# Optimization experiments

Hardware: AMD Instinct MI355X
Metric: run time of the kernel (lower is better)

## Reference

```python
import jax, jax.numpy as jnp
import numpy as np

D_IN, D_HEAD, D_EXPAND, D_OUT, H = 512, 64, 2048, 512, 8
D_Q = D_HEAD * H  # 512
D_K = D_HEAD * H  # 512
D_V = D_IN * H    # 4096 (non-standard: per-head value dim = d_in)
EPS = 1e-5


def layernorm(x, g, b):
    mu = jnp.mean(x, axis=-1, keepdims=True)
    var = jnp.mean(jnp.square(x - mu), axis=-1, keepdims=True)
    return (x - mu) * jax.lax.rsqrt(var + EPS) * g + b


def setup_inputs() -> dict:
    key = jax.random.key(0)
    ks = jax.random.split(key, 12)
    B, N = 2, 2048
    s_in = 1.0 / np.sqrt(D_IN)
    s_mh = 1.0 / np.sqrt(D_IN * H)
    s_ex = 1.0 / np.sqrt(D_EXPAND)
    return {
        "x": jax.random.normal(ks[0], (B, N, D_IN), jnp.float32),
        "ln1_g": jnp.ones((D_IN,), jnp.float32),
        "ln1_b": jnp.zeros((D_IN,), jnp.float32),
        "Wqkv": jax.random.normal(ks[1], (D_IN, D_Q + D_K + D_V), jnp.float32) * s_in,
        "bqkv": jax.random.normal(ks[2], (D_Q + D_K + D_V,), jnp.float32) * 0.01,
        "Wm": jax.random.normal(ks[3], (D_IN * H, D_IN), jnp.float32) * s_mh,
        "bm": jax.random.normal(ks[4], (D_IN,), jnp.float32) * 0.01,
        "ln2_g": jnp.ones((D_IN,), jnp.float32),
        "ln2_b": jnp.zeros((D_IN,), jnp.float32),
        "W1": jax.random.normal(ks[5], (D_IN, D_EXPAND), jnp.float32) * s_in,
        "b1": jax.random.normal(ks[6], (D_EXPAND,), jnp.float32) * 0.01,
        "W2": jax.random.normal(ks[7], (D_EXPAND, D_OUT), jnp.float32) * s_ex,
        "b2": jax.random.normal(ks[8], (D_OUT,), jnp.float32) * 0.01,
    }


def reference(x, ln1_g, ln1_b, Wqkv, bqkv, Wm, bm, ln2_g, ln2_b, W1, b1, W2, b2):
    B, N, _ = x.shape
    scale = D_HEAD ** -0.5
    qkv = layernorm(x, ln1_g, ln1_b) @ Wqkv + bqkv
    q, k, v = jnp.split(qkv, [D_Q, D_Q + D_K], axis=-1)
    q = q.reshape(B, N, H, D_HEAD).transpose(0, 2, 1, 3)  # (B,H,N,dh)
    k = k.reshape(B, N, H, D_HEAD).transpose(0, 2, 1, 3)
    v = v.reshape(B, N, H, D_IN).transpose(0, 2, 1, 3)    # (B,H,N,d_in)
    attn = jax.nn.softmax(jnp.einsum('bhnd,bhmd->bhnm', q, k) * scale, axis=-1)
    out = jnp.einsum('bhnm,bhmc->bhnc', attn, v)          # (B,H,N,d_in)
    out = out.transpose(0, 2, 1, 3).reshape(B, N, H * D_IN)
    x2 = x + out @ Wm + bm
    h = layernorm(x2, ln2_g, ln2_b) @ W1 + b1
    h = h * jax.nn.sigmoid(h)  # Swish
    return h @ W2 + b2 + x2    # shortcut = Identity (d_in == d_out)
```

## Files before the change

### kernel.cpp

```cpp
#include <hip/hip_runtime.h>
#include <cmath>

typedef unsigned short u16;
typedef unsigned int   u32;
typedef __attribute__((ext_vector_type(8))) __bf16 bf16x8;
typedef __attribute__((ext_vector_type(4))) float  f32x4;
typedef __attribute__((ext_vector_type(8))) unsigned short u16x8;
typedef __attribute__((ext_vector_type(4))) unsigned short u16x4;

#define DEV __device__ __forceinline__

DEV float bf2f(u16 u){ union{u32 i; float f;} v; v.i=((u32)u)<<16; return v.f; }
DEV u16 f2bf(float f){ union{float f; u32 i;} v; v.f=f; u32 r=v.i+0x7fffu+((v.i>>16)&1u); return (u16)(r>>16); }

#if defined(__has_builtin) && __has_builtin(__builtin_amdgcn_global_load_lds)
DEV void gld16(const void* g, void* l){
  __builtin_amdgcn_global_load_lds((__attribute__((address_space(1))) void*)g,
                                   (__attribute__((address_space(3))) void*)l, 16, 0, 0);
}
#else
DEV void gld16(const void* g, void* l){ *(u16x8*)l = *(const u16x8*)g; }
#endif

#if defined(__has_builtin) && __has_builtin(__builtin_amdgcn_exp2f)
DEV float fexp2(float x){ return __builtin_amdgcn_exp2f(x); }
#else
DEV float fexp2(float x){ return exp2f(x); }
#endif

__global__ void detect_k(const u16* __restrict__ x, int* __restrict__ flag)
{
  if (threadIdx.x == 0 && blockIdx.x == 0){
    int sane = 0;
    for (int i = 0; i < 64; ++i){
      int e = (x[i] >> 7) & 0xFF;
      sane += (e >= 100 && e <= 150);
    }
    *flag = (sane < 56) ? 1 : 0;
  }
}

__global__ __launch_bounds__(256)
void conv_vecs(const void* a0,const void* a1,const void* a2,const void* a3,
               const void* a4,const void* a5,const void* a6,const void* a7,
               float* __restrict__ dst, const int* __restrict__ flag)
{
  int i = blockIdx.x*256 + threadIdx.x;
  if (i >= 10240) return;
  const void* src; int off;
  if      (i < 512)  { src=a0; off=i; }
  else if (i < 1024) { src=a1; off=i-512; }
  else if (i < 6144) { src=a2; off=i-1024; }
  else if (i < 6656) { src=a3; off=i-6144; }
  else if (i < 7168) { src=a4; off=i-6656; }
  else if (i < 7680) { src=a5; off=i-7168; }
  else if (i < 9728) { src=a6; off=i-7680; }
  else               { src=a7; off=i-9728; }
  dst[i] = (*flag) ? ((const float*)src)[off] : bf2f(((const u16*)src)[off]);
}

#define SWZ_SRC(c) (((c)&7) ^ (((c)>>3)&7))

template<int SWZ>
DEV void remap_xcd(int& bx, int& by)
{
  if (SWZ==1){
    int L = by*(int)gridDim.x + bx;
    int xcd = L & 7, l = L >> 3;
    int chunk = (int)gridDim.x >> 3;
    bx = xcd*chunk + (l % chunk);
    by = l / chunk;
  } else if (SWZ==2){
    int L = by*(int)gridDim.x + bx;
    int xcd = L & 7, l = L >> 3;
    int chunk = (int)gridDim.y >> 3;
    by = xcd*chunk + (l % chunk);
    bx = l / chunk;
  }
}

template<int MODE, int SWZ, bool VT>
__global__ __launch_bounds__(256)
void gemm_bt(const u16* __restrict__ A, const u16* __restrict__ BT,
             void* __restrict__ C, const float* __restrict__ bias,
             int K, int lda, int ldb, int ldc, u16* __restrict__ vout)
{
  __shared__ u16 AB[2*128*64];
  u16* As = AB;
  u16* Bs = AB + 128*64;
  const int tid  = threadIdx.x;
  const int lane = tid & 63;
  const int quad = lane>>4, l7 = lane&7, l15 = lane&15;
  const int wv   = tid >> 6;
  const int wm   = wv >> 1, wn = wv & 1;
  int bx = blockIdx.x, by = blockIdx.y;
  remap_xcd<SWZ>(bx, by);
  const long m0 = (long)by * 128;
  const long n0 = (long)bx * 128;

  f32x4 acc[4][4];
#pragma unroll
  for (int i=0;i<4;i++)
#pragma unroll
    for (int j=0;j<4;j++) acc[i][j] = (f32x4){0.f,0.f,0.f,0.f};

  for (int k0=0; k0<K; k0+=64){
    __syncthreads();
#pragma unroll
    for (int i=0;i<4;i++){
      int c = i*256 + tid;
      gld16(A  + (m0 + (c>>3))*lda + k0 + SWZ_SRC(c)*8, &As[c*8]);
      gld16(BT + (n0 + (c>>3))*ldb + k0 + SWZ_SRC(c)*8, &Bs[c*8]);
    }
    __syncthreads();
#pragma unroll
    for (int kk=0;kk<2;kk++){
      const int ch = ((kk*4 + quad) ^ l7) * 8;
      bf16x8 af[4], bfr[4];
#pragma unroll
      for (int t=0;t<4;t++){
        af[t]  = *(const bf16x8*)&As[(wm*64 + t*16 + l15)*64 + ch];
        bfr[t] = *(const bf16x8*)&Bs[(wn*64 + t*16 + l15)*64 + ch];
      }
#pragma unroll
      for (int ti=0;ti<4;ti++)
#pragma unroll
        for (int tj=0;tj<4;tj++)
          acc[ti][tj] = __builtin_amdgcn_mfma_f32_16x16x32_bf16(af[ti], bfr[tj], acc[ti][tj], 0,0,0);
    }
  }

  if (VT && n0 >= 1024){
    const int hh   = (int)((n0 - 1024) >> 9);
    const int c0   = (int)((n0 - 1024) & 511);
    const int b_   = (int)(m0 >> 11);
    const int kloc = (int)(m0 & 2047);
    u16* vb = vout + ((long)(b_*8 + hh))*512*2048 + kloc;
    u16* Ts = AB;
    __syncthreads();
#pragma unroll
    for (int pass=0; pass<2; ++pass){
      if (pass) __syncthreads();
      if (wn == pass){
#pragma unroll
        for (int ti=0;ti<4;ti++)
#pragma unroll
        for (int tj=0;tj<4;tj++)
#pragma unroll
        for (int r=0;r<4;r++){
          int row = wm*64 + ti*16 + quad*4 + r;
          int cl  = tj*16 + l15;
          float v = acc[ti][tj][r] + bias[n0 + pass*64 + cl];
          Ts[row*68 + cl] = f2bf(v);
        }
      }
      __syncthreads();
#pragma unroll
      for (int step=0; step<4; ++step){
        int cr = step*16 + (tid>>4);
        int t8 = (tid&15)*8;
        u16x8 pk;
#pragma unroll
        for (int j=0;j<8;j++) pk[j] = Ts[(t8+j)*68 + cr];
        *(u16x8*)(vb + (long)(c0 + pass*64 + cr)*2048 + t8) = pk;
      }
    }
    return;
  }

#pragma unroll
  for (int ti=0;ti<4;ti++)
#pragma unroll
  for (int tj=0;tj<4;tj++)
#pragma unroll
  for (int r=0;r<4;r++){
    long row = m0 + wm*64 + ti*16 + quad*4 + r;
    long col = n0 + wn*64 + tj*16 + l15;
    float v = acc[ti][tj][r] + bias[col];
    if (MODE==2) v = v / (1.f + __expf(-v));
    ((u16*)C)[row*ldc+col] = f2bf(v);
  }
}

template<int MODE, int SWZ>
__global__ __launch_bounds__(256)
void gemm_n64(const u16* __restrict__ A, const u16* __restrict__ BT,
              void* __restrict__ C, const float* __restrict__ bias,
              const void* __restrict__ res,
              int K, int lda, int ldb, int ldc, const int* __restrict__ flag)
{
  __shared__ u16 As[2][128*64];
  __shared__ u16 Bs[2][64*64];
  const int tid  = threadIdx.x;
  const int lane = tid & 63;
  const int quad = lane>>4, l7 = lane&7, l15 = lane&15;
  const int wm   = tid >> 6;
  int bx = blockIdx.x, by = blockIdx.y;
  remap_xcd<SWZ>(bx, by);
  const long m0 = (long)by * 128;
  const long n0 = (long)bx * 64;
  const bool f32io = flag && (*flag != 0);

  f32x4 acc[2][4];
#pragma unroll
  for (int i=0;i<2;i++)
#pragma unroll
    for (int j=0;j<4;j++) acc[i][j] = (f32x4){0.f,0.f,0.f,0.f};

  auto stage = [&](int bi, int k0){
#pragma unroll
    for (int i=0;i<4;i++){
      int c = i*256 + tid;
      gld16(A + (m0 + (c>>3))*lda + k0 + SWZ_SRC(c)*8, &As[bi][c*8]);
    }
#pragma unroll
    for (int i=0;i<2;i++){
      int c = i*256 + tid;
      gld16(BT + (n0 + (c>>3))*ldb + k0 + SWZ_SRC(c)*8, &Bs[bi][c*8]);
    }
  };

  const int S = K >> 6;
  stage(0, 0);
  __syncthreads();

  for (int s=0; s<S; ++s){
    const int cb = s & 1;
    if (s+1 < S) stage(cb^1, (s+1)<<6);
#pragma unroll
    for (int kk=0;kk<2;kk++){
      const int ch = ((kk*4 + quad) ^ l7) * 8;
      bf16x8 af[2], bfr[4];
#pragma unroll
      for (int t=0;t<2;t++)
        af[t]  = *(const bf16x8*)&As[cb][(wm*32 + t*16 + l15)*64 + ch];
#pragma unroll
      for (int t=0;t<4;t++)
        bfr[t] = *(const bf16x8*)&Bs[cb][(t*16 + l15)*64 + ch];
#pragma unroll
      for (int ti=0;ti<2;ti++)
#pragma unroll
        for (int tj=0;tj<4;tj++)
          acc[ti][tj] = __builtin_amdgcn_mfma_f32_16x16x32_bf16(af[ti], bfr[tj], acc[ti][tj], 0,0,0);
    }
    __syncthreads();
  }

#pragma unroll
  for (int ti=0;ti<2;ti++)
#pragma unroll
  for (int tj=0;tj<4;tj++)
#pragma unroll
  for (int r=0;r<4;r++){
    long row = m0 + wm*32 + ti*16 + quad*4 + r;
    long col = n0 + tj*16 + l15;
    float v = acc[ti][tj][r] + bias[col];
    if (MODE==1){
      v += f32io ? ((const float*)res)[row*ldc+col]
                 : bf2f(((const u16*)res)[row*ldc+col]);
      ((float*)C)[row*ldc+col] = v;
    } else {
      v += ((const float*)res)[row*ldc+col];
      if (f32io) ((float*)C)[row*ldc+col] = v;
      else       ((u16*)C)[row*ldc+col]   = f2bf(v);
    }
  }
}

__global__ __launch_bounds__(512, 2)
void att_flash(const u16* __restrict__ qkv, const u16* __restrict__ vt,
               u16* __restrict__ ao)
{
  __shared__ u16 Qs[128*64];
  __shared__ u16 Ks[2][64*64];
  __shared__ u16 Ps[128*68];
  __shared__ u16 Vs[512*64];
  __shared__ float m_run[128], l_run[128], alph[128];
  __shared__ int resc[2];
  const int tid=threadIdx.x, lane=tid&63, wv=tid>>6;
  const int wm=wv>>2, wn=wv&3;
  const int quad=lane>>4, l7=lane&7, l15=lane&15;
  const int bid = blockIdx.x;
  const int id  = ((bid&7)<<5) + (bid>>3);
  const int qt  = id & 15, bh = id >> 4;
  const int b = bh>>3, h = bh&7;
  const long q0 = (long)qt*128;
  const u16* qb = qkv + ((long)b*2048 + q0)*5120 + h*64;
  const u16* kb = qkv + (long)b*2048*5120 + 512 + h*64;
  const u16* vb = vt + (long)bh*512*2048;

#pragma unroll
  for (int i=0;i<2;i++){
    int c=i*512+tid;
    gld16(qb + (long)(c>>3)*5120 + SWZ_SRC(c)*8, &Qs[c*8]);
  }
  { int c=tid; gld16(kb + (long)(c>>3)*5120 + SWZ_SRC(c)*8, &Ks[0][c*8]); }
  if (tid<128){ m_run[tid] = -1e30f; l_run[tid] = 0.f; }
  if (tid==0){ resc[0]=0; resc[1]=0; }

  f32x4 o[4][8];
#pragma unroll
  for (int i=0;i<4;i++)
#pragma unroll
    for (int j=0;j<8;j++) o[i][j] = (f32x4){0.f,0.f,0.f,0.f};

  __syncthreads();
  bf16x8 qreg[2];
#pragma unroll
  for (int kk=0;kk<2;kk++)
    qreg[kk] = *(const bf16x8*)&Qs[(wv*16 + l15)*64 + ((kk*4 + quad) ^ l7)*8];

  for (int mt=0; mt<32; ++mt){
    const long m0 = (long)mt*64;
    const int cur = mt&1;
    __syncthreads();

    if (mt < 31){ int c=tid; gld16(kb + (m0+64 + (c>>3))*5120 + SWZ_SRC(c)*8, &Ks[cur^1][c*8]); }
#pragma unroll
    for (int i=0;i<8;i++){
      int c=i*512+tid;
      gld16(vb + (long)(c>>3)*2048 + m0 + SWZ_SRC(c)*8, &Vs[c*8]);
    }
    if (tid==0) resc[cur^1] = 0;

    f32x4 s[4];
#pragma unroll
    for (int j=0;j<4;j++) s[j] = (f32x4){0.f,0.f,0.f,0.f};
#pragma unroll
    for (int kk=0;kk<2;kk++){
      const int ch = ((kk*4 + quad) ^ l7) * 8;
#pragma unroll
      for (int tj=0;tj<4;tj++){
        bf16x8 bfr = *(const bf16x8*)&Ks[cur][(tj*16 + l15)*64 + ch];
        s[tj] = __builtin_amdgcn_mfma_f32_16x16x32_bf16(qreg[kk], bfr, s[tj], 0,0,0);
      }
    }

    float nm[4], al[4], rs[4];
    bool chg = false;
#pragma unroll
    for (int r=0;r<4;r++){
      float vm = fmaxf(fmaxf(s[0][r],s[1][r]), fmaxf(s[2][r],s[3][r]));
      vm = fmaxf(vm, __shfl_xor(vm,1)); vm = fmaxf(vm, __shfl_xor(vm,2));
      vm = fmaxf(vm, __shfl_xor(vm,4)); vm = fmaxf(vm, __shfl_xor(vm,8));
      float mo = m_run[wv*16 + quad*4 + r];
      float vs = vm*0.125f;
      bool c_ = (vs > mo + 8.f);
      nm[r] = c_ ? vs : mo;
      al[r] = c_ ? __expf(mo - vs) : 1.f;
      chg |= c_;
      rs[r] = 0.f;
    }
    float nml[4];
#pragma unroll
    for (int r=0;r<4;r++) nml[r] = nm[r]*1.44269504f;
#pragma unroll
    for (int tj=0;tj<4;tj++)
#pragma unroll
    for (int r=0;r<4;r++){
      float pv = fexp2(fmaf(s[tj][r], 0.18033688f, -nml[r]));
      rs[r] += pv;
      Ps[(wv*16 + quad*4 + r)*68 + tj*16 + l15] = f2bf(pv);
    }
#pragma unroll
    for (int r=0;r<4;r++){
      rs[r] += __shfl_xor(rs[r],1); rs[r] += __shfl_xor(rs[r],2);
      rs[r] += __shfl_xor(rs[r],4); rs[r] += __shfl_xor(rs[r],8);
    }
    if (l15==0){
#pragma unroll
      for (int r=0;r<4;r++){
        int row = wv*16 + quad*4 + r;
        alph[row]  = al[r];
        m_run[row] = nm[r];
        l_run[row] = l_run[row]*al[r] + rs[r];
      }
    }
    if (__any((int)chg) && lane==0) resc[cur] = 1;
    __syncthreads();

    if (resc[cur]){
      float a_[4][4];
#pragma unroll
      for (int ti=0;ti<4;ti++)
#pragma unroll
        for (int r=0;r<4;r++) a_[ti][r] = alph[wm*64 + ti*16 + quad*4 + r];
#pragma unroll
      for (int ti=0;ti<4;ti++)
#pragma unroll
      for (int tj=0;tj<8;tj++)
#pragma unroll
        for (int r=0;r<4;r++) o[ti][tj][r] *= a_[ti][r];
    }
#pragma unroll
    for (int kk=0;kk<2;kk++){
      const int ch = ((kk*4 + quad) ^ l7) * 8;
      bf16x8 af[4], bfr[8];
#pragma unroll
      for (int t=0;t<4;t++){
        int base = (wm*64 + t*16 + l15)*68 + kk*32 + quad*8;
        union { u16x4 hh[2]; bf16x8 v; } u;
        u.hh[0] = *(const u16x4*)&Ps[base];
        u.hh[1] = *(const u16x4*)&Ps[base+4];
        af[t] = u.v;
      }
#pragma unroll
      for (int t=0;t<8;t++)
        bfr[t] = *(const bf16x8*)&Vs[(wn*128 + t*16 + l15)*64 + ch];
#pragma unroll
      for (int ti=0;ti<4;ti++)
#pragma unroll
        for (int tj=0;tj<8;tj++)
          o[ti][tj] = __builtin_amdgcn_mfma_f32_16x16x32_bf16(af[ti], bfr[tj], o[ti][tj], 0,0,0);
    }
  }

  float rl[4][4];
#pragma unroll
  for (int ti=0;ti<4;ti++)
#pragma unroll
    for (int r=0;r<4;r++) rl[ti][r] = 1.f / l_run[wm*64 + ti*16 + quad*4 + r];
#pragma unroll
  for (int ti=0;ti<4;ti++)
#pragma unroll
  for (int tj=0;tj<8;tj++)
#pragma unroll
  for (int r=0;r<4;r++){
    long rown = q0 + wm*64 + ti*16 + quad*4 + r;
    long col  = wn*128 + tj*16 + l15;
    ao[((long)b*2048 + rown)*4096 + (long)h*512 + col] = f2bf(o[ti][tj][r]*rl[ti][r]);
  }
}

template<int SRC>
__global__ __launch_bounds__(256)
void ln_kernel(const void* __restrict__ xin, const float* __restrict__ g,
               const float* __restrict__ bb, u16* __restrict__ out,
               const int* __restrict__ flag)
{
  const int tid=threadIdx.x, lane=tid&63, wv=tid>>6;
  const long row = (long)blockIdx.x*4 + wv;
  const bool f32 = (SRC==1) || (flag && *flag != 0);
  float v[8];
  if (f32){
    const float* xr = (const float*)xin + row*512 + lane*8;
#pragma unroll
    for (int j=0;j<8;j++) v[j]=xr[j];
  } else {
    const u16* xr = (const u16*)xin + row*512 + lane*8;
    u16x8 xv = *(const u16x8*)xr;
#pragma unroll
    for (int j=0;j<8;j++) v[j]=bf2f(xv[j]);
  }
  float s1=0.f, s2=0.f;
#pragma unroll
  for (int j=0;j<8;j++){ s1+=v[j]; s2+=v[j]*v[j]; }
  for (int off=1; off<64; off<<=1){ s1+=__shfl_xor(s1,off); s2+=__shfl_xor(s2,off); }
  float mu  = s1*(1.f/512.f);
  float var = s2*(1.f/512.f) - mu*mu;
  float rs  = rsqrtf(var + 1e-5f);
  u16x8 ov;
#pragma unroll
  for (int j=0;j<8;j++){
    int col = lane*8+j;
    ov[j] = f2bf((v[j]-mu)*rs*g[col] + bb[col]);
  }
  *(u16x8*)(out + row*512 + lane*8) = ov;
}

template<bool DUAL>
__global__ __launch_bounds__(256)
void transpose_k(const void* __restrict__ in_, u16* __restrict__ out,
                 int ldi, int ldo, long izh, long izl, long oz,
                 const int* __restrict__ flag)
{
  __shared__ u16 t[32][33];
  const int z = blockIdx.z;
  const bool f32 = DUAL && flag && (*flag != 0);
  const long zoff = (long)(z>>3)*izh + (long)(z&7)*izl;
  out += (long)z*oz;
  const int tx = threadIdx.x, ty = threadIdx.y;
  const long c  = (long)blockIdx.x*32 + tx;
  const long r0 = (long)blockIdx.y*32;
  if (f32){
    const float* in = (const float*)in_ + zoff;
#pragma unroll
    for (int j=0;j<4;j++) t[ty+j*8][tx] = f2bf(in[(r0+ty+j*8)*ldi + c]);
  } else {
    const u16* in = (const u16*)in_ + zoff;
#pragma unroll
    for (int j=0;j<4;j++) t[ty+j*8][tx] = in[(r0+ty+j*8)*ldi + c];
  }
  __syncthreads();
  const long rr = r0 + tx;
  const long cc = (long)blockIdx.x*32 + ty;
#pragma unroll
  for (int j=0;j<4;j++) out[(cc+j*8)*ldo + rr] = t[tx][ty+j*8];
}

extern "C" void kernel_launch(void* const* d_in, const int* in_sizes, int n_in,
                              void* d_out, int out_size, void* d_ws, size_t ws_size,
                              hipStream_t stream)
{
  const void* x    = d_in[0];
  const void* ln1g = d_in[1];
  const void* ln1b = d_in[2];
  const void* Wqkv = d_in[3];
  const void* bqkv = d_in[4];
  const void* Wm   = d_in[5];
  const void* bm   = d_in[6];
  const void* ln2g = d_in[7];
  const void* ln2b = d_in[8];
  const void* W1   = d_in[9];
  const void* b1   = d_in[10];
  const void* W2   = d_in[11];
  const void* b2   = d_in[12];

  char* p = (char*)d_ws;
  auto take = [&](size_t n){ void* r=(void*)p; p += (n + 255) & ~(size_t)255; return r; };
  u16*   lnb   = (u16*)  take((size_t)4096*512*2);
  u16*   qkv   = (u16*)  take((size_t)4096*5120*2);
  u16*   vtb   = (u16*)  take((size_t)16*512*2048*2);
  u16*   wqkvT = (u16*)  take((size_t)5120*512*2);
  u16*   wmT   = (u16*)  take((size_t)512*4096*2);
  u16*   w1T   = (u16*)  take((size_t)2048*512*2);
  u16*   w2T   = (u16*)  take((size_t)512*2048*2);
  u16*   ao    = (u16*)  take((size_t)4096*4096*2);
  float* cvec  = (float*)take((size_t)10240*4);
  int*   flag  = (int*)  take(4);
  float* x2    = (float*)vtb;
  u16*   hb    = qkv;

  detect_k<<<1, 64, 0, stream>>>((const u16*)x, flag);
  conv_vecs<<<40, 256, 0, stream>>>(ln1g, ln1b, bqkv, bm, ln2g, ln2b, b1, b2, cvec, flag);

  dim3 tb(32,8);
  transpose_k<true><<<dim3(160,16,1), tb, 0, stream>>>(Wqkv, wqkvT, 5120, 512, 0,0,0, flag);
  transpose_k<true><<<dim3(16,128,1), tb, 0, stream>>>(Wm,   wmT,   512, 4096, 0,0,0, flag);
  transpose_k<true><<<dim3(64,16,1),  tb, 0, stream>>>(W1,   w1T,  2048, 512, 0,0,0, flag);
  transpose_k<true><<<dim3(16,64,1),  tb, 0, stream>>>(W2,   w2T,   512, 2048, 0,0,0, flag);

  ln_kernel<0><<<1024, 256, 0, stream>>>(x, cvec+0, cvec+512, lnb, flag);
  gemm_bt<0,1,true><<<dim3(40,32), 256, 0, stream>>>(lnb, wqkvT, qkv, cvec+1024,
                                                     512, 512, 512, 5120, vtb);

  att_flash<<<dim3(256), 512, 0, stream>>>(qkv, vtb, ao);

  gemm_n64<1,2><<<dim3(8,32), 256, 0, stream>>>(ao, wmT, x2, cvec+6144, x,
                                                4096, 4096, 4096, 512, flag);
  ln_kernel<1><<<1024, 256, 0, stream>>>(x2, cvec+6656, cvec+7168, lnb, nullptr);
  gemm_bt<2,2,false><<<dim3(16,32), 256, 0, stream>>>(lnb, w1T, hb, cvec+7680,
                                                      512, 512, 512, 2048, nullptr);
  gemm_n64<3,2><<<dim3(8,32), 256, 0, stream>>>(hb, w2T, d_out, cvec+9728, x2,
                                                2048, 2048, 2048, 512, flag);
}
```

Baseline: 388.1 us.

## Software-pipeline flash attention PV with double-buffered tiles; widen n64 GEMM to 512 threads

The attention kernel now uses 32-key tiles with double-buffered K, V and P in LDS. The P·V product for the previous tile runs after the QK^T of the current tile, so only one barrier is needed per iteration. Running max and sum move into registers, Q is loaded straight from global into registers, and V gets a new XOR swizzle, which cuts LDS use. The n64 GEMM goes from 4 to 8 waves per block, each wave computing 16 rows, to raise per-block parallelism at the cost of less register reuse of the B fragments. The cost is twice as many loop iterations with smaller MFMA batches and a three-slot rescale flag scheme that is more complex to get right.

```diff
diff --git a/kernel.cpp b/kernel.cpp
--- a/kernel.cpp
+++ b/kernel.cpp
@@ -183,7 +183,7 @@
 }
 
 template<int MODE, int SWZ>
-__global__ __launch_bounds__(256)
+__global__ __launch_bounds__(512)
 void gemm_n64(const u16* __restrict__ A, const u16* __restrict__ BT,
               void* __restrict__ C, const float* __restrict__ bias,
               const void* __restrict__ res,
@@ -201,23 +201,18 @@
   const long n0 = (long)bx * 64;
   const bool f32io = flag && (*flag != 0);
 
-  f32x4 acc[2][4];
-#pragma unroll
-  for (int i=0;i<2;i++)
-#pragma unroll
-    for (int j=0;j<4;j++) acc[i][j] = (f32x4){0.f,0.f,0.f,0.f};
+  f32x4 acc[4];
+#pragma unroll
+  for (int j=0;j<4;j++) acc[j] = (f32x4){0.f,0.f,0.f,0.f};
 
   auto stage = [&](int bi, int k0){
 #pragma unroll
-    for (int i=0;i<4;i++){
-      int c = i*256 + tid;
+    for (int i=0;i<2;i++){
+      int c = i*512 + tid;
       gld16(A + (m0 + (c>>3))*lda + k0 + SWZ_SRC(c)*8, &As[bi][c*8]);
     }
-#pragma unroll
-    for (int i=0;i<2;i++){
-      int c = i*256 + tid;
-      gld16(BT + (n0 + (c>>3))*ldb + k0 + SWZ_SRC(c)*8, &Bs[bi][c*8]);
-    }
+    { int c = tid;
+      gld16(BT + (n0 + (c>>3))*ldb + k0 + SWZ_SRC(c)*8, &Bs[bi][c*8]); }
   };
 
   const int S = K >> 6;
@@ -230,31 +225,25 @@
 #pragma unroll
     for (int kk=0;kk<2;kk++){
       const int ch = ((kk*4 + quad) ^ l7) * 8;
-      bf16x8 af[2], bfr[4];
-#pragma unroll
-      for (int t=0;t<2;t++)
-        af[t]  = *(const bf16x8*)&As[cb][(wm*32 + t*16 + l15)*64 + ch];
+      bf16x8 af = *(const bf16x8*)&As[cb][(wm*16 + l15)*64 + ch];
+      bf16x8 bfr[4];
 #pragma unroll
       for (int t=0;t<4;t++)
         bfr[t] = *(const bf16x8*)&Bs[cb][(t*16 + l15)*64 + ch];
 #pragma unroll
-      for (int ti=0;ti<2;ti++)
-#pragma unroll
-        for (int tj=0;tj<4;tj++)
-          acc[ti][tj] = __builtin_amdgcn_mfma_f32_16x16x32_bf16(af[ti], bfr[tj], acc[ti][tj], 0,0,0);
+      for (int tj=0;tj<4;tj++)
+        acc[tj] = __builtin_amdgcn_mfma_f32_16x16x32_bf16(af, bfr[tj], acc[tj], 0,0,0);
     }
     __syncthreads();
   }
 
 #pragma unroll
-  for (int ti=0;ti<2;ti++)
-#pragma unroll
   for (int tj=0;tj<4;tj++)
 #pragma unroll
   for (int r=0;r<4;r++){
-    long row = m0 + wm*32 + ti*16 + quad*4 + r;
+    long row = m0 + wm*16 + quad*4 + r;
     long col = n0 + tj*16 + l15;
-    float v = acc[ti][tj][r] + bias[col];
+    float v = acc[tj][r] + bias[col];
     if (MODE==1){
       v += f32io ? ((const float*)res)[row*ldc+col]
                  : bf2f(((const u16*)res)[row*ldc+col]);
@@ -271,12 +260,12 @@
 void att_flash(const u16* __restrict__ qkv, const u16* __restrict__ vt,
                u16* __restrict__ ao)
 {
-  __shared__ u16 Qs[128*64];
-  __shared__ u16 Ks[2][64*64];
-  __shared__ u16 Ps[128*68];
-  __shared__ u16 Vs[512*64];
-  __shared__ float m_run[128], l_run[128], alph[128];
-  __shared__ int resc[2];
+  __shared__ u16 Ks[2][32*64];
+  __shared__ u16 Ps[2][128*36];
+  __shared__ u16 Vs[2][512*32];
+  __shared__ float alph[2][128];
+  __shared__ float l_lds[128];
+  __shared__ int resc[3];
   const int tid=threadIdx.x, lane=tid&63, wv=tid>>6;
   const int wm=wv>>2, wn=wv&3;
   const int quad=lane>>4, l7=lane&7, l15=lane&15;
@@ -289,14 +278,17 @@
   const u16* kb = qkv + (long)b*2048*5120 + 512 + h*64;
   const u16* vb = vt + (long)bh*512*2048;
 
-#pragma unroll
-  for (int i=0;i<2;i++){
-    int c=i*512+tid;
-    gld16(qb + (long)(c>>3)*5120 + SWZ_SRC(c)*8, &Qs[c*8]);
-  }
-  { int c=tid; gld16(kb + (long)(c>>3)*5120 + SWZ_SRC(c)*8, &Ks[0][c*8]); }
-  if (tid<128){ m_run[tid] = -1e30f; l_run[tid] = 0.f; }
-  if (tid==0){ resc[0]=0; resc[1]=0; }
+  bf16x8 qreg[2];
+#pragma unroll
+  for (int kk=0;kk<2;kk++)
+    qreg[kk] = *(const bf16x8*)(qb + (long)(wv*16 + l15)*5120 + (kk*4+quad)*8);
+
+  if (tid < 256){ int c=tid; gld16(kb + (long)(c>>3)*5120 + SWZ_SRC(c)*8, &Ks[0][c*8]); }
+  if (tid < 3) resc[tid] = 0;
+
+  float m_run[4], l_run[4];
+#pragma unroll
+  for (int r=0;r<4;r++){ m_run[r] = -1e30f; l_run[r] = 0.f; }
 
   f32x4 o[4][8];
 #pragma unroll
@@ -304,122 +296,126 @@
 #pragma unroll
     for (int j=0;j<8;j++) o[i][j] = (f32x4){0.f,0.f,0.f,0.f};
 
+  auto do_pv = [&](int pb, int rslot){
+    if (resc[rslot]){
+      float a_[4][4];
+#pragma unroll
+      for (int ti=0;ti<4;ti++)
+#pragma unroll
+        for (int r=0;r<4;r++) a_[ti][r] = alph[pb][wm*64 + ti*16 + quad*4 + r];
+#pragma unroll
+      for (int ti=0;ti<4;ti++)
+#pragma unroll
+      for (int tj=0;tj<8;tj++)
+#pragma unroll
+        for (int r=0;r<4;r++) o[ti][tj][r] *= a_[ti][r];
+    }
+    bf16x8 paf[4], pbf[8];
+#pragma unroll
+    for (int t=0;t<4;t++){
+      int base = (wm*64 + t*16 + l15)*36 + quad*8;
+      union { u16x4 hh[2]; bf16x8 v; } u;
+      u.hh[0] = *(const u16x4*)&Ps[pb][base];
+      u.hh[1] = *(const u16x4*)&Ps[pb][base+4];
+      paf[t] = u.v;
+    }
+#pragma unroll
+    for (int t=0;t<8;t++){
+      int cr = wn*128 + t*16 + l15;
+      int p  = (quad ^ (cr&3) ^ ((cr>>2)&3)) * 8;
+      pbf[t] = *(const bf16x8*)&Vs[pb][cr*32 + p];
+    }
+#pragma unroll
+    for (int ti=0;ti<4;ti++)
+#pragma unroll
+      for (int tj=0;tj<8;tj++)
+        o[ti][tj] = __builtin_amdgcn_mfma_f32_16x16x32_bf16(paf[ti], pbf[tj], o[ti][tj], 0,0,0);
+  };
+
   __syncthreads();
-  bf16x8 qreg[2];
-#pragma unroll
-  for (int kk=0;kk<2;kk++)
-    qreg[kk] = *(const bf16x8*)&Qs[(wv*16 + l15)*64 + ((kk*4 + quad) ^ l7)*8];
-
-  for (int mt=0; mt<32; ++mt){
-    const long m0 = (long)mt*64;
-    const int cur = mt&1;
-    __syncthreads();
-
-    if (mt < 31){ int c=tid; gld16(kb + (m0+64 + (c>>3))*5120 + SWZ_SRC(c)*8, &Ks[cur^1][c*8]); }
-#pragma unroll
-    for (int i=0;i<8;i++){
-      int c=i*512+tid;
-      gld16(vb + (long)(c>>3)*2048 + m0 + SWZ_SRC(c)*8, &Vs[c*8]);
-    }
-    if (tid==0) resc[cur^1] = 0;
-
-    f32x4 s[4];
-#pragma unroll
-    for (int j=0;j<4;j++) s[j] = (f32x4){0.f,0.f,0.f,0.f};
+
+  for (int mt=0; mt<64; ++mt){
+    const int cur = mt & 1;
+    const long m0 = (long)mt*32;
+
+#pragma unroll
+    for (int i=0;i<4;i++){
+      int c = i*512 + tid, row = c>>2, k4 = c&3;
+      int src = k4 ^ (row&3) ^ ((row>>2)&3);
+      gld16(vb + (long)row*2048 + m0 + src*8, &Vs[cur][c*8]);
+    }
+    if (mt < 63 && tid < 256){
+      int c = tid;
+      gld16(kb + (m0+32 + (c>>3))*5120 + SWZ_SRC(c)*8, &Ks[cur^1][c*8]);
+    }
+    if (tid==0) resc[(mt+1)%3] = 0;
+
+    f32x4 s[2];
+    s[0] = (f32x4){0.f,0.f,0.f,0.f}; s[1] = (f32x4){0.f,0.f,0.f,0.f};
 #pragma unroll
     for (int kk=0;kk<2;kk++){
       const int ch = ((kk*4 + quad) ^ l7) * 8;
 #pragma unroll
-      for (int tj=0;tj<4;tj++){
+      for (int tj=0;tj<2;tj++){
         bf16x8 bfr = *(const bf16x8*)&Ks[cur][(tj*16 + l15)*64 + ch];
         s[tj] = __builtin_amdgcn_mfma_f32_16x16x32_bf16(qreg[kk], bfr, s[tj], 0,0,0);
       }
     }
 
-    float nm[4], al[4], rs[4];
+    if (mt) do_pv(cur^1, (mt+2)%3);
+
+    float nm[4], al[4], rsum[4];
     bool chg = false;
 #pragma unroll
     for (int r=0;r<4;r++){
-      float vm = fmaxf(fmaxf(s[0][r],s[1][r]), fmaxf(s[2][r],s[3][r]));
+      float vm = fmaxf(s[0][r], s[1][r]);
       vm = fmaxf(vm, __shfl_xor(vm,1)); vm = fmaxf(vm, __shfl_xor(vm,2));
       vm = fmaxf(vm, __shfl_xor(vm,4)); vm = fmaxf(vm, __shfl_xor(vm,8));
-      float mo = m_run[wv*16 + quad*4 + r];
       float vs = vm*0.125f;
-      bool c_ = (vs > mo + 8.f);
-      nm[r] = c_ ? vs : mo;
-      al[r] = c_ ? __expf(mo - vs) : 1.f;
+      bool c_ = (vs > m_run[r] + 8.f);
+      nm[r] = c_ ? vs : m_run[r];
+      al[r] = c_ ? __expf(m_run[r] - vs) : 1.f;
       chg |= c_;
-      rs[r] = 0.f;
+      rsum[r] = 0.f;
     }
     float nml[4];
 #pragma unroll
     for (int r=0;r<4;r++) nml[r] = nm[r]*1.44269504f;
 #pragma unroll
-    for (int tj=0;tj<4;tj++)
+    for (int tj=0;tj<2;tj++)
 #pragma unroll
     for (int r=0;r<4;r++){
       float pv = fexp2(fmaf(s[tj][r], 0.18033688f, -nml[r]));
-      rs[r] += pv;
-      Ps[(wv*16 + quad*4 + r)*68 + tj*16 + l15] = f2bf(pv);
+      rsum[r] += pv;
+      Ps[cur][(wv*16 + quad*4 + r)*36 + tj*16 + l15] = f2bf(pv);
     }
 #pragma unroll
     for (int r=0;r<4;r++){
-      rs[r] += __shfl_xor(rs[r],1); rs[r] += __shfl_xor(rs[r],2);
-      rs[r] += __shfl_xor(rs[r],4); rs[r] += __shfl_xor(rs[r],8);
+      rsum[r] += __shfl_xor(rsum[r],1); rsum[r] += __shfl_xor(rsum[r],2);
+      rsum[r] += __shfl_xor(rsum[r],4); rsum[r] += __shfl_xor(rsum[r],8);
+      l_run[r] = l_run[r]*al[r] + rsum[r];
+      m_run[r] = nm[r];
     }
     if (l15==0){
 #pragma unroll
-      for (int r=0;r<4;r++){
-        int row = wv*16 + quad*4 + r;
-        alph[row]  = al[r];
-        m_run[row] = nm[r];
-        l_run[row] = l_run[row]*al[r] + rs[r];
-      }
-    }
-    if (__any((int)chg) && lane==0) resc[cur] = 1;
+      for (int r=0;r<4;r++) alph[cur][wv*16 + quad*4 + r] = al[r];
+    }
+    if (__any((int)chg) && lane==0) resc[mt%3] = 1;
+
     __syncthreads();
-
-    if (resc[cur]){
-      float a_[4][4];
-#pragma unroll
-      for (int ti=0;ti<4;ti++)
-#pragma unroll
-        for (int r=0;r<4;r++) a_[ti][r] = alph[wm*64 + ti*16 + quad*4 + r];
-#pragma unroll
-      for (int ti=0;ti<4;ti++)
-#pragma unroll
-      for (int tj=0;tj<8;tj++)
-#pragma unroll
-        for (int r=0;r<4;r++) o[ti][tj][r] *= a_[ti][r];
-    }
-#pragma unroll
-    for (int kk=0;kk<2;kk++){
-      const int ch = ((kk*4 + quad) ^ l7) * 8;
-      bf16x8 af[4], bfr[8];
-#pragma unroll
-      for (int t=0;t<4;t++){
-        int base = (wm*64 + t*16 + l15)*68 + kk*32 + quad*8;
-        union { u16x4 hh[2]; bf16x8 v; } u;
-        u.hh[0] = *(const u16x4*)&Ps[base];
-        u.hh[1] = *(const u16x4*)&Ps[base+4];
-        af[t] = u.v;
-      }
-#pragma unroll
-      for (int t=0;t<8;t++)
-        bfr[t] = *(const bf16x8*)&Vs[(wn*128 + t*16 + l15)*64 + ch];
-#pragma unroll
-      for (int ti=0;ti<4;ti++)
-#pragma unroll
-        for (int tj=0;tj<8;tj++)
-          o[ti][tj] = __builtin_amdgcn_mfma_f32_16x16x32_bf16(af[ti], bfr[tj], o[ti][tj], 0,0,0);
-    }
-  }
-
+  }
+
+  do_pv(1, 63%3);
+  if (l15==0){
+#pragma unroll
+    for (int r=0;r<4;r++) l_lds[wv*16 + quad*4 + r] = l_run[r];
+  }
+  __syncthreads();
   float rl[4][4];
 #pragma unroll
   for (int ti=0;ti<4;ti++)
 #pragma unroll
-    for (int r=0;r<4;r++) rl[ti][r] = 1.f / l_run[wm*64 + ti*16 + quad*4 + r];
+    for (int r=0;r<4;r++) rl[ti][r] = 1.f / l_lds[wm*64 + ti*16 + quad*4 + r];
 #pragma unroll
   for (int ti=0;ti<4;ti++)
 #pragma unroll
@@ -546,11 +542,11 @@
 
   att_flash<<<dim3(256), 512, 0, stream>>>(qkv, vtb, ao);
 
-  gemm_n64<1,2><<<dim3(8,32), 256, 0, stream>>>(ao, wmT, x2, cvec+6144, x,
+  gemm_n64<1,2><<<dim3(8,32), 512, 0, stream>>>(ao, wmT, x2, cvec+6144, x,
                                                 4096, 4096, 4096, 512, flag);
   ln_kernel<1><<<1024, 256, 0, stream>>>(x2, cvec+6656, cvec+7168, lnb, nullptr);
   gemm_bt<2,2,false><<<dim3(16,32), 256, 0, stream>>>(lnb, w1T, hb, cvec+7680,
                                                       512, 512, 512, 2048, nullptr);
-  gemm_n64<3,2><<<dim3(8,32), 256, 0, stream>>>(hb, w2T, d_out, cvec+9728, x2,
+  gemm_n64<3,2><<<dim3(8,32), 512, 0, stream>>>(hb, w2T, d_out, cvec+9728, x2,
                                                 2048, 2048, 2048, 512, flag);
 }
```

Result: slower. 403.8 us (+4.0%).
